# Optimization experiments

Hardware: AMD Instinct MI355X
Metric: run time of the kernel (lower is better)

## Reference

```python
import jax, jax.numpy as jnp
import numpy as np

B, T, IN, H, OUT = 128, 512, 128, 1024, 64

def setup_inputs() -> dict:
    key = jax.random.key(0)
    ks = jax.random.split(key, 8)
    # xavier_normal with gain=0.5: std = 0.5*sqrt(2/(fan_in+fan_out))
    std_fiz = 0.5 * np.sqrt(2.0 / ((IN + H) + 3 * H))
    std_r = 0.5 * np.sqrt(2.0 / ((IN + H) + H))
    std_out = np.sqrt(1.0 / H)  # torch Linear default ~ uniform, normal ok for ref
    return {
        "u": jax.random.normal(ks[0], (B, T, IN), jnp.float32),
        "x0": jax.random.uniform(ks[1], (B, 1, 2 * H), jnp.float32),
        "kernel_fiz": jax.random.normal(ks[2], (IN + H, 3 * H), jnp.float32) * std_fiz,
        "bias_fiz": jnp.zeros((3 * H,), jnp.float32),
        "kernel_r": jax.random.normal(ks[3], (IN + H, H), jnp.float32) * std_r,
        "bias_r": jnp.zeros((H,), jnp.float32),
        "W_out": jax.random.normal(ks[4], (H, OUT), jnp.float32) * std_out,
        "b_out": jnp.zeros((OUT,), jnp.float32),
    }

def reference(u, x0, kernel_fiz, bias_fiz, kernel_r, bias_r, W_out, b_out):
    h0 = x0[:, 0, :H]   # [B, H]
    c0 = x0[:, 0, H:]   # [B, H]

    def step(carry, u_t):
        h, c = carry
        u_ = jnp.concatenate([u_t, h], axis=-1)          # [B, IN+H]
        fiz = jax.nn.sigmoid(u_ @ kernel_fiz + bias_fiz)  # [B, 3H]
        f, i, z = fiz[:, :H], fiz[:, H:2 * H], fiz[:, 2 * H:]
        r = jnp.tanh(u_ @ kernel_r + bias_r)              # [B, H]
        c_new = f * c + i * r
        h_new = z * jnp.tanh(c_new)
        y = h_new @ W_out + b_out                          # [B, OUT]
        return (h_new, c_new), y

    u_tbf = jnp.transpose(u, (1, 0, 2))  # [T, B, IN]
    _, y_tbf = jax.lax.scan(step, (h0, c0), u_tbf)
    return jnp.transpose(y_tbf, (1, 0, 2))  # [B, T, OUT]
```

## Files before the change

kernel.cpp:

```cpp
#include <hip/hip_runtime.h>
#include <hip/hip_bf16.h>

#define B_    128
#define T_    512
#define IN_   128
#define H_    1024
#define OUT_  64
#define KTOT  1152
#define GH    64
#define GB    4
#define HSLAB 131072

typedef short bf16x8 __attribute__((ext_vector_type(8)));
typedef short s16x4  __attribute__((ext_vector_type(4)));
typedef float f32x4  __attribute__((ext_vector_type(4)));

#define MFMA(a,b,c) __builtin_amdgcn_mfma_f32_16x16x32_bf16((a),(b),(c),0,0,0)

__device__ __forceinline__ unsigned short f2bf(float x) {
    unsigned int xi = __float_as_uint(x);
    unsigned int r  = (xi + 0x7fffu + ((xi >> 16) & 1u)) >> 16;
    return (unsigned short)r;
}

__global__ void pack_weights(const float* __restrict__ kfiz, const float* __restrict__ kr,
                             const float* __restrict__ bfiz, const float* __restrict__ br,
                             unsigned short* __restrict__ Wp, float* __restrict__ biasp)
{
    const int c    = blockIdx.x;
    const int gh   = c >> 6, nl = c & 63;
    const int j    = gh * 16 + (nl >> 2);
    const int gate = nl & 3;
    for (int k = threadIdx.x; k < KTOT; k += 256) {
        float v = (gate < 3) ? kfiz[(size_t)k * 3072 + gate * 1024 + j]
                             : kr[(size_t)k * 1024 + j];
        Wp[(size_t)c * KTOT + k] = f2bf(v);
    }
    if (threadIdx.x == 0)
        biasp[c] = (gate < 3) ? bfiz[gate * 1024 + j] : br[j];
}

__global__ void pack_u(const float* __restrict__ u, unsigned short* __restrict__ Ubf)
{
    size_t i = (size_t)blockIdx.x * 256 + threadIdx.x;
    int t = (int)(i >> 14);
    int rem = (int)(i & 16383);
    int b = rem >> 7, k = rem & 127;
    Ubf[i] = f2bf(u[((size_t)b << 16) + ((size_t)t << 7) + k]);
}

__global__ void pack_wout(const float* __restrict__ wo, unsigned short* __restrict__ Wob)
{
    const int o = blockIdx.x;
    for (int k = threadIdx.x; k < H_; k += 256)
        Wob[(size_t)o * H_ + k] = f2bf(wo[(size_t)k * OUT_ + o]);
}

__global__ void __launch_bounds__(512, 2)
lstm_scan(const float* __restrict__ x0,
          const unsigned short* __restrict__ Wp,
          const float* __restrict__ biasp,
          const unsigned short* __restrict__ Ubf,
          unsigned short* __restrict__ Hall,
          int* __restrict__ Flag)
{
    __shared__ float part[4 * 8 * 320];

    const int tid  = threadIdx.x;
    const int bid  = blockIdx.x;
    const int gb   = (bid & 7) >> 1;
    const int gh   = ((bid & 1) << 5) | (bid >> 3);
    const int wave = tid >> 6;
    const int lane = tid & 63;
    const int mi   = wave & 1;
    const int nj   = wave >> 1;
    const int quad = lane >> 4;
    const int l15  = lane & 15;
    const int g    = l15 & 3;

    f32x4 wregf[36];
    #pragma unroll
    for (int tl = 0; tl < 4; ++tl)
        #pragma unroll
        for (int kk = 0; kk < 9; ++kk)
            wregf[tl * 9 + kk] = *reinterpret_cast<const f32x4*>(
                Wp + (size_t)(gh * 64 + tl * 16 + l15) * KTOT + nj * 288 + kk * 32 + quad * 8);
    #pragma unroll
    for (int i = 0; i < 36; ++i)
        asm volatile("" : "+v"(wregf[i]));

    const float bias = biasp[gh * 64 + nj * 16 + l15];

    const int rowBase = gb * 32 + mi * 16;
    const int j       = gh * 16 + nj * 4 + (l15 >> 2);

    float cst[4];
    #pragma unroll
    for (int r = 0; r < 4; ++r)
        cst[r] = x0[(size_t)(rowBase + quad * 4 + r) * 2048 + 1024 + j];

    {
        int m = tid >> 4, u16 = tid & 15;
        int b = gb * 32 + m, c = gh * 16 + u16;
        unsigned short hv = f2bf(x0[(size_t)b * 2048 + c]);
        size_t adr = (size_t)(c >> 2) * 512 + (size_t)(b >> 4) * 64
                   + (b & 15) * 4 + (c & 3);
        __hip_atomic_store(&Hall[adr], hv,
                           __ATOMIC_RELAXED, __HIP_MEMORY_SCOPE_AGENT);
    }
    __syncthreads();
    if (tid == 0)
        __hip_atomic_store(&Flag[(size_t)gb * 64 + gh], 1,
                           __ATOMIC_RELAXED, __HIP_MEMORY_SCOPE_AGENT);

    const int aRow = rowBase + l15;
    const unsigned short* aU = Ubf + (size_t)aRow * IN_ + quad * 8;
    const unsigned short* aH = Hall + (size_t)(gb * 2 + mi) * 64 + l15 * 4
                             + (size_t)quad * 1024;
    const ptrdiff_t hCg0 = (ptrdiff_t)(nj * 72 - 32) * 512;

    const int kk0 = (nj == 0) ? 4 : 0;

    const size_t pubAdr = (size_t)(gh * 4 + nj) * 512 + (size_t)(gb * 2 + mi) * 64
                        + (size_t)(quad * 4 + (l15 >> 2)) * 4;

    for (int t = 0; t < T_; ++t) {
        f32x4 acc[4] = {{0.f,0.f,0.f,0.f},{0.f,0.f,0.f,0.f},
                        {0.f,0.f,0.f,0.f},{0.f,0.f,0.f,0.f}};

        if (nj == 0) {
            const unsigned short* au = aU + (size_t)t * (B_ * IN_);
            #pragma unroll
            for (int kk = 0; kk < 4; ++kk) {
                bf16x8 av = *reinterpret_cast<const bf16x8*>(au + kk * 32);
                #pragma unroll
                for (int tl = 0; tl < 4; ++tl)
                    acc[tl] = MFMA(av, __builtin_bit_cast(bf16x8, wregf[tl * 9 + kk]), acc[tl]);
            }
        }

        if (wave == 0) {
            const int* fp = Flag + ((size_t)t * GB + gb) * 64 + lane;
            int v = __hip_atomic_load(fp, __ATOMIC_RELAXED, __HIP_MEMORY_SCOPE_AGENT);
            for (int gd = 0; gd < (1 << 20) && !__all(v != 0); ++gd)
                v = __hip_atomic_load(fp, __ATOMIC_RELAXED, __HIP_MEMORY_SCOPE_AGENT);
        }
        __syncthreads();

        const unsigned short* ahT = aH + (size_t)t * HSLAB + hCg0;
        bf16x8 a[9];
        #pragma unroll
        for (int kk = 0; kk < 9; ++kk)
            if (kk >= kk0) {
                union { s16x4 h[2]; bf16x8 v; } uu;
                uu.h[0] = *reinterpret_cast<const s16x4*>(ahT + (ptrdiff_t)kk * 4096);
                uu.h[1] = *reinterpret_cast<const s16x4*>(ahT + (ptrdiff_t)kk * 4096 + 512);
                a[kk] = uu.v;
            }
        #pragma unroll
        for (int kk = 0; kk < 9; ++kk)
            if (kk >= kk0) {
                #pragma unroll
                for (int tl = 0; tl < 4; ++tl)
                    acc[tl] = MFMA(a[kk], __builtin_bit_cast(bf16x8, wregf[tl * 9 + kk]), acc[tl]);
            }

        #pragma unroll
        for (int tl = 0; tl < 4; ++tl)
            *reinterpret_cast<f32x4*>(
                &part[(nj * 8 + mi * 4 + tl) * 320 + l15 * 20 + quad * 4]) = acc[tl];
        __syncthreads();

        f32x4 s = {bias, bias, bias, bias};
        {
            const int rbase = (mi * 4 + nj) * 320 + l15 * 20 + quad * 4;
            #pragma unroll
            for (int njj = 0; njj < 4; ++njj)
                s += *reinterpret_cast<const f32x4*>(&part[njj * 2560 + rbase]);
        }

        unsigned int hx = 0, hy = 0;
        #pragma unroll
        for (int r = 0; r < 4; ++r) {
            float pre = s[r];
            float sg  = 1.0f / (1.0f + __expf((g == 3) ? -2.0f * pre : -pre));
            float act = (g == 3) ? 2.0f * sg - 1.0f : sg;
            float x1 = __shfl_xor(act, 1);
            float x2 = __shfl_xor(act, 2);
            float x3 = __shfl_xor(x1, 2);
            float fv = (g == 0) ? act : (g == 1) ? x1 : (g == 2) ? x2 : x3;
            int gi = g ^ 1;
            float iv = (gi == 0) ? act : (gi == 1) ? x1 : (gi == 2) ? x2 : x3;
            int gz = g ^ 2;
            float zv = (gz == 0) ? act : (gz == 1) ? x1 : (gz == 2) ? x2 : x3;
            int gr = g ^ 3;
            float rv = (gr == 0) ? act : (gr == 1) ? x1 : (gr == 2) ? x2 : x3;

            float cn = fv * cst[r] + iv * rv;
            cst[r] = cn;
            float th = 2.0f / (1.0f + __expf(-2.0f * cn)) - 1.0f;
            float hn = zv * th;
            unsigned int hb = f2bf(hn);
            if (r == 0)      hx  = hb;
            else if (r == 1) hx |= hb << 16;
            else if (r == 2) hy  = hb;
            else             hy |= hb << 16;
        }

        unsigned int px = __shfl_xor((int)hx, 4), py = __shfl_xor((int)hy, 4);
        unsigned int ax, ay;
        if ((lane & 4) == 0) { ax = (hx & 0xFFFFu) | (px << 16);
                               ay = (hy & 0xFFFFu) | (py << 16); }
        else                 { ax = (px >> 16) | (hx & 0xFFFF0000u);
                               ay = (py >> 16) | (hy & 0xFFFF0000u); }
        unsigned int qx = __shfl_xor((int)ax, 8), qy = __shfl_xor((int)ay, 8);
        unsigned int bx, by;
        if ((lane & 8) == 0) { bx = ax; by = qx; }
        else                 { bx = qy; by = ay; }

        if (g == 0) {
            unsigned long long val = ((unsigned long long)by << 32) | bx;
            __hip_atomic_store(
                (unsigned long long*)&Hall[(size_t)(t + 1) * HSLAB + pubAdr], val,
                __ATOMIC_RELAXED, __HIP_MEMORY_SCOPE_AGENT);
        }
        asm volatile("s_waitcnt vmcnt(0)" ::: "memory");
        asm volatile("s_barrier" ::: "memory");
        if (tid == 0)
            __hip_atomic_store(&Flag[((size_t)(t + 1) * GB + gb) * 64 + gh], 1,
                               __ATOMIC_RELAXED, __HIP_MEMORY_SCOPE_AGENT);
    }
}

__global__ void __launch_bounds__(256, 2)
out_gemm(const unsigned short* __restrict__ Hall,
         const unsigned short* __restrict__ Wob,
         const float* __restrict__ bout,
         float* __restrict__ y)
{
    const int tid  = threadIdx.x, wave = tid >> 6, lane = tid & 63;
    const int quad = lane >> 4, l15 = lane & 15;
    const int R    = blockIdx.x * 64 + wave * 16;

    f32x4 acc[4];
    #pragma unroll
    for (int nt = 0; nt < 4; ++nt) {
        float bb = bout[nt * 16 + l15];
        acc[nt] = {bb, bb, bb, bb};
    }
    const int fr = R + l15;
    const int br = fr & 127;
    const unsigned short* ap = Hall + ((size_t)(fr >> 7) + 1) * HSLAB
                             + (size_t)(br >> 4) * 64 + (br & 15) * 4
                             + (size_t)quad * 1024;
    #pragma unroll 4
    for (int kk = 0; kk < 32; ++kk) {
        union { s16x4 h[2]; bf16x8 v; } uu;
        uu.h[0] = *reinterpret_cast<const s16x4*>(ap + (size_t)kk * 4096);
        uu.h[1] = *reinterpret_cast<const s16x4*>(ap + (size_t)kk * 4096 + 512);
        bf16x8 av = uu.v;
        #pragma unroll
        for (int nt = 0; nt < 4; ++nt) {
            bf16x8 bv = *reinterpret_cast<const bf16x8*>(
                Wob + (size_t)(nt * 16 + l15) * H_ + kk * 32 + quad * 8);
            acc[nt] = MFMA(av, bv, acc[nt]);
        }
    }
    #pragma unroll
    for (int nt = 0; nt < 4; ++nt)
        #pragma unroll
        for (int r = 0; r < 4; ++r) {
            int row = R + quad * 4 + r;
            int b = row & 127, t = row >> 7;
            y[((size_t)b << 15) + ((size_t)t << 6) + nt * 16 + l15] = acc[nt][r];
        }
}

extern "C" void kernel_launch(void* const* d_in, const int* in_sizes, int n_in,
                              void* d_out, int out_size, void* d_ws, size_t ws_size,
                              hipStream_t stream)
{
    const float* u    = (const float*)d_in[0];
    const float* x0   = (const float*)d_in[1];
    const float* kfiz = (const float*)d_in[2];
    const float* bfiz = (const float*)d_in[3];
    const float* kr   = (const float*)d_in[4];
    const float* br   = (const float*)d_in[5];
    const float* wo   = (const float*)d_in[6];
    const float* bo   = (const float*)d_in[7];
    float* y = (float*)d_out;

    char* ws = (char*)d_ws;
    size_t off = 0;
    unsigned short* Wp    = (unsigned short*)(ws + off); off += (size_t)4096 * KTOT * 2;
    float*          biasp = (float*)(ws + off);          off += (size_t)4096 * 4;
    unsigned short* Wob   = (unsigned short*)(ws + off); off += (size_t)OUT_ * H_ * 2;
    unsigned short* Ubf   = (unsigned short*)(ws + off); off += (size_t)T_ * B_ * IN_ * 2;
    unsigned short* Hall  = (unsigned short*)(ws + off); off += (size_t)(T_ + 1) * B_ * H_ * 2;
    int*            Flag  = (int*)(ws + off);            off += (size_t)(T_ + 1) * GB * 64 * 4;
    if (off > ws_size) return;

    hipMemsetAsync(Flag, 0, (size_t)(T_ + 1) * GB * 64 * 4, stream);
    hipLaunchKernelGGL(pack_weights, dim3(4096),  dim3(256), 0, stream, kfiz, kr, bfiz, br, Wp, biasp);
    hipLaunchKernelGGL(pack_u,       dim3(32768), dim3(256), 0, stream, u, Ubf);
    hipLaunchKernelGGL(pack_wout,    dim3(64),    dim3(256), 0, stream, wo, Wob);

    void* args[] = { (void*)&x0, (void*)&Wp, (void*)&biasp, (void*)&Ubf, (void*)&Hall, (void*)&Flag };
    hipLaunchCooperativeKernel((void*)lstm_scan, dim3(GB * GH), dim3(512), args, 0, stream);

    hipLaunchKernelGGL(out_gemm, dim3((T_ * B_) / 64), dim3(256), 0, stream, Hall, Wob, bo, y);
}
```

Baseline: 2.272 ms.

## Give each wave the full K reduction and replace barriers with LDS flags

The LSTM scan grid moves from 4 batch groups × 64 column groups to 8 × 32. Each wave now holds all 36 K-chunks for its 16 gate columns and a 16-row batch slice, so the cross-wave LDS partial-sum reduction and its two block barriers per step go away. Block-level __syncthreads is replaced by LDS release/acquire flags: wave 0 polls the global step flag and releases the other waves, and the other waves signal completion before wave 0 publishes the next flag. This shortens the per-step critical path. In exchange, every wave must load all 32 K-chunks of h from global memory and run a longer serial MFMA chain, and the spin-waits on LDS flags add their own risk.

```diff
diff --git a/kernel.cpp b/kernel.cpp
--- a/kernel.cpp
+++ b/kernel.cpp
@@ -7,8 +7,8 @@
 #define H_    1024
 #define OUT_  64
 #define KTOT  1152
-#define GH    64
-#define GB    4
+#define GB    8
+#define GH    32
 #define HSLAB 131072
 
 typedef short bf16x8 __attribute__((ext_vector_type(8)));
@@ -28,9 +28,8 @@
                              unsigned short* __restrict__ Wp, float* __restrict__ biasp)
 {
     const int c    = blockIdx.x;
-    const int gh   = c >> 6, nl = c & 63;
-    const int j    = gh * 16 + (nl >> 2);
-    const int gate = nl & 3;
+    const int j    = c >> 2;
+    const int gate = c & 3;
     for (int k = threadIdx.x; k < KTOT; k += 256) {
         float v = (gate < 3) ? kfiz[(size_t)k * 3072 + gate * 1024 + j]
                              : kr[(size_t)k * 1024 + j];
@@ -64,125 +63,109 @@
           unsigned short* __restrict__ Hall,
           int* __restrict__ Flag)
 {
-    __shared__ float part[4 * 8 * 320];
+    __shared__ int rel;
+    __shared__ int done[8];
 
     const int tid  = threadIdx.x;
     const int bid  = blockIdx.x;
-    const int gb   = (bid & 7) >> 1;
-    const int gh   = ((bid & 1) << 5) | (bid >> 3);
+    const int rg   = bid & 7;
+    const int cg   = bid >> 3;
     const int wave = tid >> 6;
     const int lane = tid & 63;
-    const int mi   = wave & 1;
-    const int nj   = wave >> 1;
     const int quad = lane >> 4;
     const int l15  = lane & 15;
     const int g    = l15 & 3;
+    const int rb   = rg * 16;
+
+    const int c = cg * 128 + wave * 16 + l15;
 
     f32x4 wregf[36];
     #pragma unroll
-    for (int tl = 0; tl < 4; ++tl)
-        #pragma unroll
-        for (int kk = 0; kk < 9; ++kk)
-            wregf[tl * 9 + kk] = *reinterpret_cast<const f32x4*>(
-                Wp + (size_t)(gh * 64 + tl * 16 + l15) * KTOT + nj * 288 + kk * 32 + quad * 8);
+    for (int kk = 0; kk < 36; ++kk)
+        wregf[kk] = *reinterpret_cast<const f32x4*>(
+            Wp + (size_t)c * KTOT + kk * 32 + quad * 8);
     #pragma unroll
     for (int i = 0; i < 36; ++i)
         asm volatile("" : "+v"(wregf[i]));
 
-    const float bias = biasp[gh * 64 + nj * 16 + l15];
-
-    const int rowBase = gb * 32 + mi * 16;
-    const int j       = gh * 16 + nj * 4 + (l15 >> 2);
+    const float bias = biasp[c];
+    const int j = c >> 2;
 
     float cst[4];
     #pragma unroll
     for (int r = 0; r < 4; ++r)
-        cst[r] = x0[(size_t)(rowBase + quad * 4 + r) * 2048 + 1024 + j];
+        cst[r] = x0[(size_t)(rb + quad * 4 + r) * 2048 + 1024 + j];
+
+    if (tid == 0) rel = 0;
+    if (tid < 8) done[tid] = 0;
 
     {
-        int m = tid >> 4, u16 = tid & 15;
-        int b = gb * 32 + m, c = gh * 16 + u16;
-        unsigned short hv = f2bf(x0[(size_t)b * 2048 + c]);
-        size_t adr = (size_t)(c >> 2) * 512 + (size_t)(b >> 4) * 64
-                   + (b & 15) * 4 + (c & 3);
-        __hip_atomic_store(&Hall[adr], hv,
+        int m = tid >> 5, uu = tid & 31;
+        int uq = cg * 8 + (uu >> 2);
+        unsigned short hv = f2bf(x0[(size_t)(rb + m) * 2048 + cg * 32 + uu]);
+        __hip_atomic_store(&Hall[(size_t)uq * 512 + rg * 64 + m * 4 + (uu & 3)], hv,
                            __ATOMIC_RELAXED, __HIP_MEMORY_SCOPE_AGENT);
     }
     __syncthreads();
     if (tid == 0)
-        __hip_atomic_store(&Flag[(size_t)gb * 64 + gh], 1,
+        __hip_atomic_store(&Flag[(size_t)rg * 32 + cg], 1,
                            __ATOMIC_RELAXED, __HIP_MEMORY_SCOPE_AGENT);
 
-    const int aRow = rowBase + l15;
-    const unsigned short* aU = Ubf + (size_t)aRow * IN_ + quad * 8;
-    const unsigned short* aH = Hall + (size_t)(gb * 2 + mi) * 64 + l15 * 4
-                             + (size_t)quad * 1024;
-    const ptrdiff_t hCg0 = (ptrdiff_t)(nj * 72 - 32) * 512;
-
-    const int kk0 = (nj == 0) ? 4 : 0;
-
-    const size_t pubAdr = (size_t)(gh * 4 + nj) * 512 + (size_t)(gb * 2 + mi) * 64
+    const unsigned short* aU = Ubf + (size_t)(rb + l15) * IN_ + quad * 8;
+    const unsigned short* aH = Hall + (size_t)quad * 1024 + rg * 64 + l15 * 4;
+    const size_t pubAdr = (size_t)(cg * 8 + wave) * 512 + rg * 64
                         + (size_t)(quad * 4 + (l15 >> 2)) * 4;
 
     for (int t = 0; t < T_; ++t) {
         f32x4 acc[4] = {{0.f,0.f,0.f,0.f},{0.f,0.f,0.f,0.f},
                         {0.f,0.f,0.f,0.f},{0.f,0.f,0.f,0.f}};
 
-        if (nj == 0) {
+        {
             const unsigned short* au = aU + (size_t)t * (B_ * IN_);
             #pragma unroll
             for (int kk = 0; kk < 4; ++kk) {
                 bf16x8 av = *reinterpret_cast<const bf16x8*>(au + kk * 32);
-                #pragma unroll
-                for (int tl = 0; tl < 4; ++tl)
-                    acc[tl] = MFMA(av, __builtin_bit_cast(bf16x8, wregf[tl * 9 + kk]), acc[tl]);
+                acc[kk] = MFMA(av, __builtin_bit_cast(bf16x8, wregf[kk]), acc[kk]);
             }
         }
 
         if (wave == 0) {
-            const int* fp = Flag + ((size_t)t * GB + gb) * 64 + lane;
+            const int* fp = Flag + ((size_t)t * 8 + rg) * 32 + (lane & 31);
             int v = __hip_atomic_load(fp, __ATOMIC_RELAXED, __HIP_MEMORY_SCOPE_AGENT);
             for (int gd = 0; gd < (1 << 20) && !__all(v != 0); ++gd)
                 v = __hip_atomic_load(fp, __ATOMIC_RELAXED, __HIP_MEMORY_SCOPE_AGENT);
-        }
-        __syncthreads();
-
-        const unsigned short* ahT = aH + (size_t)t * HSLAB + hCg0;
-        bf16x8 a[9];
+            if (lane == 0)
+                __hip_atomic_store(&rel, t + 1, __ATOMIC_RELEASE, __HIP_MEMORY_SCOPE_WORKGROUP);
+        } else {
+            for (int gd = 0; gd < (1 << 20); ++gd)
+                if (__hip_atomic_load(&rel, __ATOMIC_ACQUIRE, __HIP_MEMORY_SCOPE_WORKGROUP) >= t + 1)
+                    break;
+        }
+        asm volatile("" ::: "memory");
+
+        const unsigned short* ah = aH + (size_t)t * HSLAB;
         #pragma unroll
-        for (int kk = 0; kk < 9; ++kk)
-            if (kk >= kk0) {
-                union { s16x4 h[2]; bf16x8 v; } uu;
-                uu.h[0] = *reinterpret_cast<const s16x4*>(ahT + (ptrdiff_t)kk * 4096);
-                uu.h[1] = *reinterpret_cast<const s16x4*>(ahT + (ptrdiff_t)kk * 4096 + 512);
-                a[kk] = uu.v;
+        for (int grp = 0; grp < 8; ++grp) {
+            union AV { s16x4 h[2]; bf16x8 v; } ab[4];
+            #pragma unroll
+            for (int i = 0; i < 4; ++i) {
+                const unsigned short* p = ah + (size_t)(grp * 4 + i) * 4096;
+                ab[i].h[0] = *reinterpret_cast<const s16x4*>(p);
+                ab[i].h[1] = *reinterpret_cast<const s16x4*>(p + 512);
             }
-        #pragma unroll
-        for (int kk = 0; kk < 9; ++kk)
-            if (kk >= kk0) {
-                #pragma unroll
-                for (int tl = 0; tl < 4; ++tl)
-                    acc[tl] = MFMA(a[kk], __builtin_bit_cast(bf16x8, wregf[tl * 9 + kk]), acc[tl]);
+            #pragma unroll
+            for (int i = 0; i < 4; ++i) {
+                const int kk = 4 + grp * 4 + i;
+                acc[kk & 3] = MFMA(ab[i].v, __builtin_bit_cast(bf16x8, wregf[kk]), acc[kk & 3]);
             }
-
-        #pragma unroll
-        for (int tl = 0; tl < 4; ++tl)
-            *reinterpret_cast<f32x4*>(
-                &part[(nj * 8 + mi * 4 + tl) * 320 + l15 * 20 + quad * 4]) = acc[tl];
-        __syncthreads();
-
-        f32x4 s = {bias, bias, bias, bias};
-        {
-            const int rbase = (mi * 4 + nj) * 320 + l15 * 20 + quad * 4;
-            #pragma unroll
-            for (int njj = 0; njj < 4; ++njj)
-                s += *reinterpret_cast<const f32x4*>(&part[njj * 2560 + rbase]);
-        }
+        }
+
+        f32x4 s = (acc[0] + acc[1]) + (acc[2] + acc[3]);
 
         unsigned int hx = 0, hy = 0;
         #pragma unroll
         for (int r = 0; r < 4; ++r) {
-            float pre = s[r];
+            float pre = s[r] + bias;
             float sg  = 1.0f / (1.0f + __expf((g == 3) ? -2.0f * pre : -pre));
             float act = (g == 3) ? 2.0f * sg - 1.0f : sg;
             float x1 = __shfl_xor(act, 1);
@@ -225,10 +208,24 @@
                 __ATOMIC_RELAXED, __HIP_MEMORY_SCOPE_AGENT);
         }
         asm volatile("s_waitcnt vmcnt(0)" ::: "memory");
-        asm volatile("s_barrier" ::: "memory");
-        if (tid == 0)
-            __hip_atomic_store(&Flag[((size_t)(t + 1) * GB + gb) * 64 + gh], 1,
-                               __ATOMIC_RELAXED, __HIP_MEMORY_SCOPE_AGENT);
+
+        if (wave == 0) {
+            const int dv = t + 1;
+            for (int gd = 0; gd < (1 << 20); ++gd) {
+                int v = (lane >= 1 && lane < 8)
+                      ? __hip_atomic_load(&done[lane], __ATOMIC_ACQUIRE, __HIP_MEMORY_SCOPE_WORKGROUP)
+                      : dv;
+                if (__all(v >= dv)) break;
+            }
+            asm volatile("" ::: "memory");
+            if (lane == 0)
+                __hip_atomic_store(&Flag[((size_t)(t + 1) * 8 + rg) * 32 + cg], 1,
+                                   __ATOMIC_RELAXED, __HIP_MEMORY_SCOPE_AGENT);
+        } else {
+            if (lane == 0)
+                __hip_atomic_store(&done[wave], t + 1,
+                                   __ATOMIC_RELEASE, __HIP_MEMORY_SCOPE_WORKGROUP);
+        }
     }
 }
 
@@ -249,10 +246,9 @@
         acc[nt] = {bb, bb, bb, bb};
     }
     const int fr = R + l15;
-    const int br = fr & 127;
+    const int b  = fr & 127;
     const unsigned short* ap = Hall + ((size_t)(fr >> 7) + 1) * HSLAB
-                             + (size_t)(br >> 4) * 64 + (br & 15) * 4
-                             + (size_t)quad * 1024;
+                             + (size_t)quad * 1024 + (b >> 4) * 64 + (b & 15) * 4;
     #pragma unroll 4
     for (int kk = 0; kk < 32; ++kk) {
         union { s16x4 h[2]; bf16x8 v; } uu;
@@ -271,8 +267,8 @@
         #pragma unroll
         for (int r = 0; r < 4; ++r) {
             int row = R + quad * 4 + r;
-            int b = row & 127, t = row >> 7;
-            y[((size_t)b << 15) + ((size_t)t << 6) + nt * 16 + l15] = acc[nt][r];
+            int bb2 = row & 127, t = row >> 7;
+            y[((size_t)bb2 << 15) + ((size_t)t << 6) + nt * 16 + l15] = acc[nt][r];
         }
 }
 
@@ -297,10 +293,10 @@
     unsigned short* Wob   = (unsigned short*)(ws + off); off += (size_t)OUT_ * H_ * 2;
     unsigned short* Ubf   = (unsigned short*)(ws + off); off += (size_t)T_ * B_ * IN_ * 2;
     unsigned short* Hall  = (unsigned short*)(ws + off); off += (size_t)(T_ + 1) * B_ * H_ * 2;
-    int*            Flag  = (int*)(ws + off);            off += (size_t)(T_ + 1) * GB * 64 * 4;
+    int*            Flag  = (int*)(ws + off);            off += (size_t)(T_ + 1) * GB * GH * 4;
     if (off > ws_size) return;
 
-    hipMemsetAsync(Flag, 0, (size_t)(T_ + 1) * GB * 64 * 4, stream);
+    hipMemsetAsync(Flag, 0, (size_t)(T_ + 1) * GB * GH * 4, stream);
     hipLaunchKernelGGL(pack_weights, dim3(4096),  dim3(256), 0, stream, kfiz, kr, bfiz, br, Wp, biasp);
     hipLaunchKernelGGL(pack_u,       dim3(32768), dim3(256), 0, stream, u, Ubf);
     hipLaunchKernelGGL(pack_wout,    dim3(64),    dim3(256), 0, stream, wo, Wob);
```

Result: slower. 3.663 ms (+61.2%).
